# Kernel optimization log

Measured on AMD Instinct MI355X. Metric: run time of the kernel, lower is better.

## Reference

```python
import jax, jax.numpy as jnp
import numpy as np

TOP_K = 5
TRUNC = 100
EPS = 1e-07
B, T_STEPS, I_DIM, H_DIM, N_CLS = 32, 384, 64, 128, 10


def setup_inputs() -> dict:
    key = jax.random.key(0)
    ks = jax.random.split(key, 8)
    s = 1.0 / np.sqrt(H_DIM)
    u = lambda k, sh: jax.random.uniform(k, sh, jnp.float32, -s, s)
    return {
        "x": jax.random.normal(ks[0], (B, T_STEPS, I_DIM), jnp.float32),
        "W_ih": u(ks[1], (4 * H_DIM, I_DIM)),
        "W_hh": u(ks[2], (4 * H_DIM, H_DIM)),
        "b_ih": u(ks[3], (4 * H_DIM,)),
        "b_hh": u(ks[4], (4 * H_DIM,)),
        "w_t": jax.random.normal(ks[5], (2 * H_DIM, 1), jnp.float32) * 0.01,
        "W_fc": u(ks[6], (N_CLS, 2 * H_DIM)),
        "b_fc": u(ks[7], (N_CLS,)),
    }


def _lstm_cell(x_t, h, c, W_ih, W_hh, b_ih, b_hh):
    # torch.nn.LSTMCell: gate order i, f, g, o
    g = x_t @ W_ih.T + b_ih + h @ W_hh.T + b_hh
    i, f, gg, o = jnp.split(g, 4, axis=1)
    c = jax.nn.sigmoid(f) * c + jax.nn.sigmoid(i) * jnp.tanh(gg)
    h = jax.nn.sigmoid(o) * jnp.tanh(c)
    return h, c


def _sparse_attn(scores, mask, r):
    # scores: [B, T+1]; mask: valid-prefix bool [T+1]; r: traced valid length
    Bsz, L = scores.shape
    neg = jnp.where(mask[None, :], scores, -jnp.inf)

    def small(_):
        return jax.nn.softmax(neg, axis=1)

    def big(_):
        delta = jax.lax.top_k(neg, TOP_K)[0][:, -1] + EPS  # [B], k-th largest
        # faithful to torch: delta.repeat((1, r)).view(B, r) -> delta[(b*r+t) % B]
        dmat = delta[(jnp.arange(Bsz)[:, None] * r + jnp.arange(L)[None, :]) % Bsz]
        w = jnp.clip(scores - dmat, 0.0, None) * mask[None, :]
        return w / (jnp.sum(w, axis=1, keepdims=True) + EPS)

    return jax.lax.cond(r <= TOP_K, small, big, None)


def reference(x, W_ih, W_hh, b_ih, b_hh, w_t, W_fc, b_fc):
    Bsz, T, _ = x.shape
    H = W_hh.shape[1]
    dt = x.dtype
    buf0 = jnp.zeros((Bsz, T + 1, H), dt)  # h_old buffer; slot 0 (zeros) is valid
    pos = jnp.arange(T + 1)

    def step(carry, inp):
        h, c, buf = carry
        i, x_t = inp
        h, c = jax.lax.cond(
            (i + 1) % TRUNC == 0,
            lambda hc: (jax.lax.stop_gradient(hc[0]), jax.lax.stop_gradient(hc[1])),
            lambda hc: hc,
            (h, c),
        )
        h, c = _lstm_cell(x_t, h, c, W_ih, W_hh, b_ih, b_hh)
        r = i + 1  # remember_size (valid prefix of buf)
        mask = (pos < r).astype(dt)  # [T+1]
        mlp = jnp.tanh(jnp.concatenate(
            (jnp.broadcast_to(h[:, None, :], buf.shape), buf), axis=2))  # [B,T+1,2H]
        scores = (mlp @ w_t)[..., 0]  # [B, T+1]
        attn = _sparse_attn(scores, mask, r)  # [B, T+1], zero on invalid slots
        attn_c = jnp.einsum('bt,bth->bh', attn, buf)
        h = h + attn_c
        buf = jax.lax.dynamic_update_slice(buf, h[:, None, :], (0, r, 0))
        return (h, c, buf), (h, attn_c)

    init = (jnp.zeros((Bsz, H), dt), jnp.zeros((Bsz, H), dt), buf0)
    _, (hs, attn_all) = jax.lax.scan(step, init, (jnp.arange(T), jnp.swapaxes(x, 0, 1)))
    outputs = jnp.concatenate(
        (jnp.swapaxes(hs, 0, 1), jnp.swapaxes(attn_all, 0, 1)), axis=2)  # [B,T,2H]
    out = outputs @ W_fc.T + b_fc  # [B, T, num_classes]
    return out, jnp.swapaxes(hs, 0, 1)
```

## Files before the change

kernel.cpp:

```cpp
#include <hip/hip_runtime.h>
#include <stdint.h>

typedef unsigned long long u64;

#define NB   32
#define TST  384
#define IDM  64
#define HDM  128
#define NCLS 10
#define EPSF 1e-7f
#define LOG2E 1.44269504088896340736f

#define O_SBUF 0
#define O_WLDS 388
#define O_ACT  776
#define O_GEX  968
#define O_RED  1480
#define O_DELT 2504
#define O_WFC  2536
#define O_BFC  5176
#define O_MISC 5188
#define SMTOT  5220

__device__ __forceinline__ float sigm(float x) {
  return 1.0f / (1.0f + __builtin_amdgcn_exp2f(-LOG2E * x));
}
__device__ __forceinline__ float tanh_f(float x) {
  return 1.0f - 2.0f / (1.0f + __builtin_amdgcn_exp2f(2.0f * LOG2E * x));
}

__device__ __forceinline__ void mail_store(u64* p, u64 v) {
  asm volatile("global_store_dwordx2 %0, %1, off sc0 sc1"
               :: "v"(p), "v"(v) : "memory");
}
__device__ __forceinline__ u64 mail_load(u64* p) {
  u64 v;
  asm volatile("global_load_dwordx2 %0, %1, off sc0 sc1\n\t"
               "s_waitcnt vmcnt(0)"
               : "=v"(v) : "v"(p) : "memory");
  return v;
}

__global__ __launch_bounds__(512, 2)
void sab_kernel(const float* __restrict__ x, const float* __restrict__ Wih,
                const float* __restrict__ Whh, const float* __restrict__ bihp,
                const float* __restrict__ bhhp, const float* __restrict__ wtp,
                const float* __restrict__ Wfcp, const float* __restrict__ bfcp,
                float* __restrict__ dout, u64* __restrict__ mail) {
  __shared__ __align__(16) float SM[SMTOT];
  int* IMISC = (int*)(SM + O_MISC);
  int* IDX   = (int*)(SM + O_GEX);

  const int tid  = threadIdx.x;
  const int lane = tid & 63;
  const int wvid = tid >> 6;
  const int b    = blockIdx.x;
  const int go   = tid >> 3;
  const int kc   = tid & 7;

  float* hsout = dout + (size_t)NB * TST * NCLS;
  const float* myx = x + (size_t)b * TST * IDM;

  float w[8][24];
  #pragma unroll
  for (int i = 0; i < 8; ++i) {
    const int g = 8 * go + i;
    #pragma unroll
    for (int j = 0; j < 24; ++j) {
      const int k = 24 * kc + j;
      const float* sp = (k < IDM) ? (Wih + g * IDM + k) : (Whh + g * HDM + (k - IDM));
      w[i][j] = *sp;
    }
  }
  const float bias = bihp[tid] + bhhp[tid];
  float wt0 = 0.f, wt1 = 0.f, cst = 0.f;
  if (tid < HDM) { wt0 = wtp[tid]; wt1 = wtp[HDM + tid]; }

  float t5a = 0.f, t5b = -3e38f, t5c = -3e38f, t5d = -3e38f, t5e = -3e38f;

  for (int idx = tid; idx < NCLS * 256; idx += 512) {
    const int c = idx >> 8, k = idx & 255;
    SM[O_WFC + c * 264 + k] = Wfcp[idx];
  }
  if (tid < NCLS) SM[O_BFC + tid] = bfcp[tid];
  if (tid < HDM) SM[O_ACT + 64 + tid] = 0.f;
  if (tid < IDM) SM[O_ACT + tid] = myx[tid];
  if (tid == 0) {
    SM[O_SBUF] = 0.f;
    mail_store(&mail[b], 0ull);
    mail_store(&mail[NB + b], 0ull);
  }
  __syncthreads();

  float hc = 0.f;
  for (int t = 0; t < TST; ++t) {
    const int r = t + 1;
    const bool big = (r > 5);

    float acc[8] = {0,0,0,0,0,0,0,0};
    {
      const float4* a4 = reinterpret_cast<const float4*>(SM + O_ACT + kc * 24);
      #pragma unroll
      for (int m = 0; m < 6; ++m) {
        const float4 av = a4[m];
        #pragma unroll
        for (int i = 0; i < 8; ++i) {
          acc[i] = fmaf(av.x, w[i][4*m+0], acc[i]);
          acc[i] = fmaf(av.y, w[i][4*m+1], acc[i]);
          acc[i] = fmaf(av.z, w[i][4*m+2], acc[i]);
          acc[i] = fmaf(av.w, w[i][4*m+3], acc[i]);
        }
      }
    }
    #pragma unroll
    for (int i = 0; i < 8; ++i) {
      acc[i] += __shfl_xor(acc[i], 1, 64);
      acc[i] += __shfl_xor(acc[i], 2, 64);
      acc[i] += __shfl_xor(acc[i], 4, 64);
    }
    float pre = acc[0];
    #pragma unroll
    for (int i = 1; i < 8; ++i) if (kc == i) pre = acc[i];
    pre += bias;
    const bool tg = (tid >= 256) && (tid < 384);
    SM[O_RED + tid] = tg ? tanh_f(pre) : sigm(pre);
    __syncthreads();

    float th = 0.f;
    if (tid < HDM) {
      const float iv = SM[O_RED + tid];
      const float fv = SM[O_RED + 128 + tid];
      const float gv = SM[O_RED + 256 + tid];
      const float ov = SM[O_RED + 384 + tid];
      cst = fv * cst + iv * gv;
      hc  = ov * tanh_f(cst);
      th  = tanh_f(hc) * wt0;
    }
    #pragma unroll
    for (int s = 1; s < 64; s <<= 1) th += __shfl_xor(th, s, 64);
    if (lane == 0 && tid < HDM) SM[O_MISC + wvid] = th;
    __syncthreads();
    const float s_h = SM[O_MISC] + SM[O_MISC + 1];

    if (big && tid == 0) {
      const float delta = t5e + s_h + EPSF;
      const u64 pv = (((u64)(unsigned)r) << 32) | (u64)__float_as_uint(delta);
      mail_store(&mail[(r & 1) * NB + b], pv);
    }

    float xr = 0.f;
    if (tid < IDM && t + 1 < TST) xr = myx[(size_t)(t + 1) * IDM + tid];
    if (t > 0 && tid < 160) {
      const int cls = tid >> 4, p = tid & 15;
      float pt = 0.f;
      #pragma unroll
      for (int i = 0; i < 16; ++i) {
        const int k = p + 16 * i;
        pt = fmaf(SM[O_WFC + cls * 264 + k], SM[O_GEX + k], pt);
      }
      #pragma unroll
      for (int s2 = 1; s2 < 16; s2 <<= 1) pt += __shfl_xor(pt, s2, 64);
      if (p == 0) dout[((size_t)(b * TST + (t - 1))) * NCLS + cls] = pt + SM[O_BFC + cls];
    }

    if (big && wvid == 7 && lane < NB) {
      u64* slot = &mail[(r & 1) * NB + lane];
      u64 v = mail_load(slot);
      while ((unsigned)(v >> 32) != (unsigned)r) {
        __builtin_amdgcn_s_sleep(2);
        v = mail_load(slot);
      }
      SM[O_DELT + lane] = __uint_as_float((unsigned)v);
    }
    __syncthreads();

    float wval = 0.f;
    bool pred = false;
    if (big) {
      if (tid < r) {
        const float sc = s_h + SM[O_SBUF + tid];
        wval = fmaxf(sc - SM[O_DELT + ((b * r + tid) & (NB - 1))], 0.f);
        SM[O_WLDS + tid] = wval;
        pred = (wval > 0.f) && (tid > 0);
      }
    } else {
      float scv = (tid < r) ? (s_h + SM[O_SBUF + tid]) : -3e38f;
      float mx = scv;
      #pragma unroll
      for (int s = 1; s < 64; s <<= 1) mx = fmaxf(mx, __shfl_xor(mx, s, 64));
      if (tid < r) {
        wval = __builtin_amdgcn_exp2f(LOG2E * (scv - mx));
        SM[O_WLDS + tid] = wval;
        pred = (tid > 0);
      }
    }
    float wsp = wval;
    #pragma unroll
    for (int s = 1; s < 64; s <<= 1) wsp += __shfl_xor(wsp, s, 64);
    if (lane == 0) SM[O_MISC + 2 + wvid] = wsp;
    const u64 bmask = __ballot((int)pred);
    if (lane == 0) IMISC[16 + wvid] = (int)__popcll(bmask);
    __syncthreads();

    float wsum = 0.f;
    #pragma unroll
    for (int i = 0; i < 8; ++i) wsum += SM[O_MISC + 2 + i];
    const float inv = 1.0f / (wsum + (big ? EPSF : 0.f));
    int wbase = 0, nnz = 0;
    #pragma unroll
    for (int i = 0; i < 8; ++i) {
      const int c = IMISC[16 + i];
      if (i < wvid) wbase += c;
      nnz += c;
    }
    if (pred) {
      const int pos = wbase + (int)__popcll(bmask & ((1ull << lane) - 1ull));
      IDX[pos] = tid;
    }
    __syncthreads();

    const int j8 = tid & 15, q = tid >> 4;
    float ac[8] = {0,0,0,0,0,0,0,0};
    for (int ii = q; ii < nnz; ii += 32) {
      const int tp = IDX[ii];
      const float wgt = SM[O_WLDS + tp] * inv;
      const float* bp = hsout + ((size_t)(b * TST + tp - 1)) * HDM + j8 * 8;
      const float4 v0 = *reinterpret_cast<const float4*>(bp);
      const float4 v1 = *reinterpret_cast<const float4*>(bp + 4);
      ac[0] = fmaf(wgt, v0.x, ac[0]); ac[1] = fmaf(wgt, v0.y, ac[1]);
      ac[2] = fmaf(wgt, v0.z, ac[2]); ac[3] = fmaf(wgt, v0.w, ac[3]);
      ac[4] = fmaf(wgt, v1.x, ac[4]); ac[5] = fmaf(wgt, v1.y, ac[5]);
      ac[6] = fmaf(wgt, v1.z, ac[6]); ac[7] = fmaf(wgt, v1.w, ac[7]);
    }
    #pragma unroll
    for (int i = 0; i < 8; ++i) {
      ac[i] += __shfl_xor(ac[i], 16, 64);
      ac[i] += __shfl_xor(ac[i], 32, 64);
    }
    if ((q & 3) == 0) {
      float4* r4 = reinterpret_cast<float4*>(SM + O_RED + wvid * 128 + j8 * 8);
      r4[0] = make_float4(ac[0], ac[1], ac[2], ac[3]);
      r4[1] = make_float4(ac[4], ac[5], ac[6], ac[7]);
    }
    __syncthreads();

    float tb = 0.f;
    if (tid < HDM) {
      float s = 0.f;
      #pragma unroll
      for (int wv2 = 0; wv2 < 8; ++wv2) s += SM[O_RED + wv2 * 128 + tid];
      const float hf = hc + s;
      hsout[((size_t)(b * TST + t)) * HDM + tid] = hf;
      SM[O_ACT + 64 + tid] = hf;
      SM[O_GEX + tid] = hf;
      SM[O_GEX + 128 + tid] = s;
      tb = tanh_f(hf) * wt1;
    }
    if (tid < IDM && t + 1 < TST) SM[O_ACT + tid] = xr;
    #pragma unroll
    for (int s2 = 1; s2 < 64; s2 <<= 1) tb += __shfl_xor(tb, s2, 64);
    if (lane == 0 && tid < HDM) SM[O_MISC + 24 + wvid] = tb;
    __syncthreads();

    if (tid == 0 && r < TST) {
      const float sb = SM[O_MISC + 24] + SM[O_MISC + 25];
      SM[O_SBUF + r] = sb;
      if (sb > t5e) {
        if (sb > t5a)      { t5e=t5d; t5d=t5c; t5c=t5b; t5b=t5a; t5a=sb; }
        else if (sb > t5b) { t5e=t5d; t5d=t5c; t5c=t5b; t5b=sb; }
        else if (sb > t5c) { t5e=t5d; t5d=t5c; t5c=sb; }
        else if (sb > t5d) { t5e=t5d; t5d=sb; }
        else               { t5e=sb; }
      }
    }
  }

  if (tid < 160) {
    const int cls = tid >> 4, p = tid & 15;
    float pt = 0.f;
    #pragma unroll
    for (int i = 0; i < 16; ++i) {
      const int k = p + 16 * i;
      pt = fmaf(SM[O_WFC + cls * 264 + k], SM[O_GEX + k], pt);
    }
    #pragma unroll
    for (int s2 = 1; s2 < 16; s2 <<= 1) pt += __shfl_xor(pt, s2, 64);
    if (p == 0) dout[((size_t)(b * TST + (TST - 1))) * NCLS + cls] = pt + SM[O_BFC + cls];
  }
}

extern "C" void kernel_launch(void* const* d_in, const int* in_sizes, int n_in,
                              void* d_out, int out_size, void* d_ws, size_t ws_size,
                              hipStream_t stream) {
  const float* x   = (const float*)d_in[0];
  const float* Wih = (const float*)d_in[1];
  const float* Whh = (const float*)d_in[2];
  const float* bih = (const float*)d_in[3];
  const float* bhh = (const float*)d_in[4];
  const float* wt  = (const float*)d_in[5];
  const float* Wfc = (const float*)d_in[6];
  const float* bfc = (const float*)d_in[7];
  sab_kernel<<<dim3(NB), dim3(512), 0, stream>>>(
      x, Wih, Whh, bih, bhh, wt, Wfc, bfc, (float*)d_out, (u64*)d_ws);
}
```

Before: 1.893 ms.

## Specialize waves per step and use DPP reductions to cut barriers

Moves the LSTM cell update, score reduction, mailbox publish and top-5 update onto wave 0, which handles two hidden units per lane. The x prefetch, mailbox polling and output FC projection run concurrently on other waves. This removes one block-wide barrier per timestep, drops the sleep in the spin loop, and folds the attention normalization into the final per-hidden sum. Butterfly shuffles are replaced with DPP row operations for the sub-16-lane reductions. The price is more serial work on wave 0 and busier spinning on the mailbox.

```diff
diff --git a/kernel.cpp b/kernel.cpp
--- a/kernel.cpp
+++ b/kernel.cpp
@@ -29,6 +29,31 @@
   return 1.0f - 2.0f / (1.0f + __builtin_amdgcn_exp2f(2.0f * LOG2E * x));
 }
 
+template <int CTRL>
+__device__ __forceinline__ float dppadd(float v) {
+  int t = __builtin_amdgcn_update_dpp(0, __builtin_bit_cast(int, v), CTRL, 0xF, 0xF, true);
+  return v + __builtin_bit_cast(float, t);
+}
+__device__ __forceinline__ float sum8(float v) {
+  v = dppadd<0xB1>(v);
+  v = dppadd<0x4E>(v);
+  v = dppadd<0x141>(v);
+  return v;
+}
+__device__ __forceinline__ float sum16(float v) {
+  v = dppadd<0xB1>(v);
+  v = dppadd<0x4E>(v);
+  v = dppadd<0x141>(v);
+  v = dppadd<0x140>(v);
+  return v;
+}
+__device__ __forceinline__ float wave_sum(float v) {
+  v = sum16(v);
+  v += __shfl_xor(v, 16, 64);
+  v += __shfl_xor(v, 32, 64);
+  return v;
+}
+
 __device__ __forceinline__ void mail_store(u64* p, u64 v) {
   asm volatile("global_store_dwordx2 %0, %1, off sc0 sc1"
                :: "v"(p), "v"(v) : "memory");
@@ -73,8 +98,13 @@
     }
   }
   const float bias = bihp[tid] + bhhp[tid];
-  float wt0 = 0.f, wt1 = 0.f, cst = 0.f;
-  if (tid < HDM) { wt0 = wtp[tid]; wt1 = wtp[HDM + tid]; }
+
+  float wt00 = 0.f, wt01 = 0.f, wt10 = 0.f, wt11 = 0.f;
+  if (wvid == 0) {
+    wt00 = wtp[lane];        wt01 = wtp[64 + lane];
+    wt10 = wtp[128 + lane];  wt11 = wtp[192 + lane];
+  }
+  float cst0 = 0.f, cst1 = 0.f, hc0 = 0.f, hc1 = 0.f;
 
   float t5a = 0.f, t5b = -3e38f, t5c = -3e38f, t5d = -3e38f, t5e = -3e38f;
 
@@ -92,7 +122,6 @@
   }
   __syncthreads();
 
-  float hc = 0.f;
   for (int t = 0; t < TST; ++t) {
     const int r = t + 1;
     const bool big = (r > 5);
@@ -113,11 +142,7 @@
       }
     }
     #pragma unroll
-    for (int i = 0; i < 8; ++i) {
-      acc[i] += __shfl_xor(acc[i], 1, 64);
-      acc[i] += __shfl_xor(acc[i], 2, 64);
-      acc[i] += __shfl_xor(acc[i], 4, 64);
-    }
+    for (int i = 0; i < 8; ++i) acc[i] = sum8(acc[i]);
     float pre = acc[0];
     #pragma unroll
     for (int i = 1; i < 8; ++i) if (kc == i) pre = acc[i];
@@ -126,53 +151,48 @@
     SM[O_RED + tid] = tg ? tanh_f(pre) : sigm(pre);
     __syncthreads();
 
-    float th = 0.f;
-    if (tid < HDM) {
-      const float iv = SM[O_RED + tid];
-      const float fv = SM[O_RED + 128 + tid];
-      const float gv = SM[O_RED + 256 + tid];
-      const float ov = SM[O_RED + 384 + tid];
-      cst = fv * cst + iv * gv;
-      hc  = ov * tanh_f(cst);
-      th  = tanh_f(hc) * wt0;
-    }
-    #pragma unroll
-    for (int s = 1; s < 64; s <<= 1) th += __shfl_xor(th, s, 64);
-    if (lane == 0 && tid < HDM) SM[O_MISC + wvid] = th;
-    __syncthreads();
-    const float s_h = SM[O_MISC] + SM[O_MISC + 1];
-
-    if (big && tid == 0) {
-      const float delta = t5e + s_h + EPSF;
-      const u64 pv = (((u64)(unsigned)r) << 32) | (u64)__float_as_uint(delta);
-      mail_store(&mail[(r & 1) * NB + b], pv);
-    }
-
-    float xr = 0.f;
-    if (tid < IDM && t + 1 < TST) xr = myx[(size_t)(t + 1) * IDM + tid];
-    if (t > 0 && tid < 160) {
-      const int cls = tid >> 4, p = tid & 15;
+    if (wvid == 0) {
+      const float i0 = SM[O_RED + lane],        i1 = SM[O_RED + 64 + lane];
+      const float f0 = SM[O_RED + 128 + lane],  f1 = SM[O_RED + 192 + lane];
+      const float g0 = SM[O_RED + 256 + lane],  g1 = SM[O_RED + 320 + lane];
+      const float o0 = SM[O_RED + 384 + lane],  o1 = SM[O_RED + 448 + lane];
+      cst0 = f0 * cst0 + i0 * g0;
+      cst1 = f1 * cst1 + i1 * g1;
+      hc0  = o0 * tanh_f(cst0);
+      hc1  = o1 * tanh_f(cst1);
+      float th = tanh_f(hc0) * wt00 + tanh_f(hc1) * wt01;
+      th = wave_sum(th);
+      if (lane == 0) {
+        SM[O_MISC] = th;
+        if (big) {
+          const u64 pv = (((u64)(unsigned)r) << 32) | (u64)__float_as_uint(t5e + th + EPSF);
+          mail_store(&mail[(r & 1) * NB + b], pv);
+        }
+      }
+    } else if (wvid == 7) {
+      if (big && lane < NB) {
+        u64* slot = &mail[(r & 1) * NB + lane];
+        u64 v = mail_load(slot);
+        while ((unsigned)(v >> 32) != (unsigned)r) v = mail_load(slot);
+        SM[O_DELT + lane] = __uint_as_float((unsigned)v);
+      }
+    } else if (wvid == 1) {
+      if (t + 1 < TST && lane < IDM)
+        SM[O_ACT + lane] = myx[(size_t)(t + 1) * IDM + lane];
+    } else if (t > 0 && tid < 288) {
+      const int cls = (tid - 128) >> 4, p = tid & 15;
       float pt = 0.f;
       #pragma unroll
       for (int i = 0; i < 16; ++i) {
         const int k = p + 16 * i;
         pt = fmaf(SM[O_WFC + cls * 264 + k], SM[O_GEX + k], pt);
       }
-      #pragma unroll
-      for (int s2 = 1; s2 < 16; s2 <<= 1) pt += __shfl_xor(pt, s2, 64);
+      pt = sum16(pt);
       if (p == 0) dout[((size_t)(b * TST + (t - 1))) * NCLS + cls] = pt + SM[O_BFC + cls];
     }
-
-    if (big && wvid == 7 && lane < NB) {
-      u64* slot = &mail[(r & 1) * NB + lane];
-      u64 v = mail_load(slot);
-      while ((unsigned)(v >> 32) != (unsigned)r) {
-        __builtin_amdgcn_s_sleep(2);
-        v = mail_load(slot);
-      }
-      SM[O_DELT + lane] = __uint_as_float((unsigned)v);
-    }
-    __syncthreads();
+    __syncthreads();
+
+    const float s_h = SM[O_MISC];
 
     float wval = 0.f;
     bool pred = false;
@@ -194,18 +214,12 @@
         pred = (tid > 0);
       }
     }
-    float wsp = wval;
-    #pragma unroll
-    for (int s = 1; s < 64; s <<= 1) wsp += __shfl_xor(wsp, s, 64);
+    const float wsp = wave_sum(wval);
     if (lane == 0) SM[O_MISC + 2 + wvid] = wsp;
     const u64 bmask = __ballot((int)pred);
     if (lane == 0) IMISC[16 + wvid] = (int)__popcll(bmask);
     __syncthreads();
 
-    float wsum = 0.f;
-    #pragma unroll
-    for (int i = 0; i < 8; ++i) wsum += SM[O_MISC + 2 + i];
-    const float inv = 1.0f / (wsum + (big ? EPSF : 0.f));
     int wbase = 0, nnz = 0;
     #pragma unroll
     for (int i = 0; i < 8; ++i) {
@@ -223,7 +237,7 @@
     float ac[8] = {0,0,0,0,0,0,0,0};
     for (int ii = q; ii < nnz; ii += 32) {
       const int tp = IDX[ii];
-      const float wgt = SM[O_WLDS + tp] * inv;
+      const float wgt = SM[O_WLDS + tp];
       const float* bp = hsout + ((size_t)(b * TST + tp - 1)) * HDM + j8 * 8;
       const float4 v0 = *reinterpret_cast<const float4*>(bp);
       const float4 v1 = *reinterpret_cast<const float4*>(bp + 4);
@@ -244,35 +258,42 @@
     }
     __syncthreads();
 
-    float tb = 0.f;
-    if (tid < HDM) {
-      float s = 0.f;
-      #pragma unroll
-      for (int wv2 = 0; wv2 < 8; ++wv2) s += SM[O_RED + wv2 * 128 + tid];
-      const float hf = hc + s;
-      hsout[((size_t)(b * TST + t)) * HDM + tid] = hf;
-      SM[O_ACT + 64 + tid] = hf;
-      SM[O_GEX + tid] = hf;
-      SM[O_GEX + 128 + tid] = s;
-      tb = tanh_f(hf) * wt1;
-    }
-    if (tid < IDM && t + 1 < TST) SM[O_ACT + tid] = xr;
-    #pragma unroll
-    for (int s2 = 1; s2 < 64; s2 <<= 1) tb += __shfl_xor(tb, s2, 64);
-    if (lane == 0 && tid < HDM) SM[O_MISC + 24 + wvid] = tb;
-    __syncthreads();
-
-    if (tid == 0 && r < TST) {
-      const float sb = SM[O_MISC + 24] + SM[O_MISC + 25];
-      SM[O_SBUF + r] = sb;
-      if (sb > t5e) {
-        if (sb > t5a)      { t5e=t5d; t5d=t5c; t5c=t5b; t5b=t5a; t5a=sb; }
-        else if (sb > t5b) { t5e=t5d; t5d=t5c; t5c=t5b; t5b=sb; }
-        else if (sb > t5c) { t5e=t5d; t5d=t5c; t5c=sb; }
-        else if (sb > t5d) { t5e=t5d; t5d=sb; }
-        else               { t5e=sb; }
-      }
-    }
+    if (wvid == 0) {
+      float wsum = 0.f;
+      #pragma unroll
+      for (int i = 0; i < 8; ++i) wsum += SM[O_MISC + 2 + i];
+      const float inv = 1.0f / (wsum + (big ? EPSF : 0.f));
+      float at0 = 0.f, at1 = 0.f;
+      #pragma unroll
+      for (int wv2 = 0; wv2 < 8; ++wv2) {
+        at0 += SM[O_RED + wv2 * 128 + lane];
+        at1 += SM[O_RED + wv2 * 128 + 64 + lane];
+      }
+      at0 *= inv; at1 *= inv;
+      const float hf0 = hc0 + at0, hf1 = hc1 + at1;
+      const size_t row = ((size_t)(b * TST + t)) * HDM;
+      hsout[row + lane]      = hf0;
+      hsout[row + 64 + lane] = hf1;
+      SM[O_ACT + 64 + lane]  = hf0;
+      SM[O_ACT + 128 + lane] = hf1;
+      SM[O_GEX + lane]       = hf0;
+      SM[O_GEX + 64 + lane]  = hf1;
+      SM[O_GEX + 128 + lane] = at0;
+      SM[O_GEX + 192 + lane] = at1;
+      float tb = tanh_f(hf0) * wt10 + tanh_f(hf1) * wt11;
+      tb = wave_sum(tb);
+      if (lane == 0 && r < TST) {
+        SM[O_SBUF + r] = tb;
+        if (tb > t5e) {
+          if (tb > t5a)      { t5e=t5d; t5d=t5c; t5c=t5b; t5b=t5a; t5a=tb; }
+          else if (tb > t5b) { t5e=t5d; t5d=t5c; t5c=t5b; t5b=tb; }
+          else if (tb > t5c) { t5e=t5d; t5d=t5c; t5c=tb; }
+          else if (tb > t5d) { t5e=t5d; t5d=tb; }
+          else               { t5e=tb; }
+        }
+      }
+    }
+    __syncthreads();
   }
 
   if (tid < 160) {
@@ -283,8 +304,7 @@
       const int k = p + 16 * i;
       pt = fmaf(SM[O_WFC + cls * 264 + k], SM[O_GEX + k], pt);
     }
-    #pragma unroll
-    for (int s2 = 1; s2 < 16; s2 <<= 1) pt += __shfl_xor(pt, s2, 64);
+    pt = sum16(pt);
     if (p == 0) dout[((size_t)(b * TST + (TST - 1))) * NCLS + cls] = pt + SM[O_BFC + cls];
   }
 }
```

Result: no change. 1.920 ms (+1.4%).
